# Performance work log

Hardware: AMD Instinct MI355X
Metric: run time of the kernel (lower is better)

## Reference

```python
import jax, jax.numpy as jnp
import numpy as np

N = 50000
E = 800000
IN_DIM = 128
HID = 64
OUT_DIM = 128
NEG_SLOPE = 0.2  # PyG GATConv default


def _add_self_loops(src, dst, edge_attr, n):
    # PyG GATConv(add_self_loops=True) with edge_dim uses fill_value='mean':
    # self-loop edge_attr = mean of edge_attr of incoming edges per node.
    deg = jax.ops.segment_sum(jnp.ones((src.shape[0],), edge_attr.dtype), dst, num_segments=n)
    loop_attr = jax.ops.segment_sum(edge_attr, dst, num_segments=n) / jnp.maximum(deg, 1.0)[:, None]
    loop = jnp.arange(n, dtype=src.dtype)
    return (jnp.concatenate([src, loop]), jnp.concatenate([dst, loop]),
            jnp.concatenate([edge_attr, loop_attr], axis=0))


def _gat_conv(x, src, dst, edge_attr, W, We, a_src, a_dst, a_edge, bias, heads, out_dim, concat, n):
    src, dst, edge_attr = _add_self_loops(src, dst, edge_attr, n)
    h = (x @ W).reshape(n, heads, out_dim)                      # [N,H,D]
    he = (edge_attr @ We).reshape(-1, heads, out_dim)           # [E',H,D]
    alpha_src = jnp.einsum('nhd,hd->nh', h, a_src)
    alpha_dst = jnp.einsum('nhd,hd->nh', h, a_dst)
    alpha_edge = jnp.einsum('ehd,hd->eh', he, a_edge)
    alpha = jax.nn.leaky_relu(alpha_src[src] + alpha_dst[dst] + alpha_edge, NEG_SLOPE)  # [E',H]
    # segment softmax over edges grouped by destination node
    amax = jax.ops.segment_max(alpha, dst, num_segments=n)
    amax = jnp.where(jnp.isfinite(amax), amax, 0.0)
    ex = jnp.exp(alpha - amax[dst])
    denom = jax.ops.segment_sum(ex, dst, num_segments=n)
    coef = ex / (denom[dst] + 1e-16)                            # [E',H]
    msg = h[src] * coef[:, :, None]                             # [E',H,D]
    out = jax.ops.segment_sum(msg, dst, num_segments=n)         # [N,H,D]
    out = out.reshape(n, heads * out_dim) if concat else out.mean(axis=1)
    return out + bias


def setup_inputs() -> dict:
    key = jax.random.key(0)
    ks = jax.random.split(key, 16)
    s = 0.05
    inp = {
        'x': jax.random.normal(ks[0], (N, IN_DIM), jnp.float32),
        'edge_index': jax.random.randint(ks[1], (2, E), 0, N, dtype=jnp.int64),
        'edge_attr': jax.random.normal(ks[2], (E, 2), jnp.float32),
        # gat1: heads=4, concat -> out 4*HID
        'W1': jax.random.normal(ks[3], (IN_DIM, 4 * HID), jnp.float32) * s,
        'We1': jax.random.normal(ks[4], (2, 4 * HID), jnp.float32) * s,
        'asrc1': jax.random.normal(ks[5], (4, HID), jnp.float32) * s,
        'adst1': jax.random.normal(ks[6], (4, HID), jnp.float32) * s,
        'aedge1': jax.random.normal(ks[7], (4, HID), jnp.float32) * s,
        'b1': jnp.zeros((4 * HID,), jnp.float32),
        # gat2: heads=1, concat=False -> out OUT_DIM
        'W2': jax.random.normal(ks[8], (4 * HID, OUT_DIM), jnp.float32) * s,
        'We2': jax.random.normal(ks[9], (2, OUT_DIM), jnp.float32) * s,
        'asrc2': jax.random.normal(ks[10], (1, OUT_DIM), jnp.float32) * s,
        'adst2': jax.random.normal(ks[11], (1, OUT_DIM), jnp.float32) * s,
        'aedge2': jax.random.normal(ks[12], (1, OUT_DIM), jnp.float32) * s,
        'b2': jnp.zeros((OUT_DIM,), jnp.float32),
    }
    return inp


def reference(x, edge_index, edge_attr, W1, We1, asrc1, adst1, aedge1, b1,
              W2, We2, asrc2, adst2, aedge2, b2):
    src, dst = edge_index[0], edge_index[1]
    # dropout layers are identity in eval mode
    h = _gat_conv(x, src, dst, edge_attr, W1, We1, asrc1, adst1, aedge1, b1,
                  heads=4, out_dim=HID, concat=True, n=x.shape[0])
    h = jax.nn.elu(h)
    out = _gat_conv(h, src, dst, edge_attr, W2, We2, asrc2, adst2, aedge2, b2,
                    heads=1, out_dim=OUT_DIM, concat=False, n=x.shape[0])
    return out
```

## Files before the change

kernel.cpp:

```cpp
#include <hip/hip_runtime.h>
#include <hip/hip_bf16.h>

#define NN 50000
#define EE 800000
#define SCAN_B 2048
#define NB ((NN + SCAN_B - 1) / SCAN_B)


typedef short bf16x8 __attribute__((ext_vector_type(8)));
typedef float f32x4  __attribute__((ext_vector_type(4)));

__device__ __forceinline__ float bf2f(unsigned short u) {
    return __uint_as_float(((unsigned)u) << 16);
}
__device__ __forceinline__ unsigned short f2bf(float f) {
    unsigned b = __float_as_uint(f);
    b += 0x7fffu + ((b >> 16) & 1u);
    return (unsigned short)(b >> 16);
}
__device__ __forceinline__ float2 bfpair(unsigned u) {
    return make_float2(__uint_as_float(u << 16), __uint_as_float(u & 0xffff0000u));
}

__global__ void k_prep(const float* __restrict__ We1, const float* __restrict__ ae1,
                       const float* __restrict__ We2, const float* __restrict__ ae2,
                       float* __restrict__ v,
                       const float* __restrict__ W1, unsigned short* __restrict__ W1t,
                       const float* __restrict__ W2, unsigned short* __restrict__ W2t,
                       const int* __restrict__ ei, int* __restrict__ idg,
                       int* __restrict__ rank,
                       const float* __restrict__ x, unsigned short* __restrict__ xb) {
    int bid = blockIdx.x, t = threadIdx.x;
    if (bid == 0) {
        if (t < 8) {
            int c = t >> 2, h = t & 3;
            float s = 0.f;
            for (int d = 0; d < 64; d++) s += We1[c * 256 + h * 64 + d] * ae1[h * 64 + d];
            v[c * 4 + h] = s;
        } else if (t < 10) {
            int c = t - 8;
            float s = 0.f;
            for (int d = 0; d < 128; d++) s += We2[c * 128 + d] * ae2[d];
            v[8 + c] = s;
        }
    } else if (bid <= 256) {
        int idx = (bid - 1) * 256 + t;
        if (idx < 32768) {
            int k = idx >> 8, n = idx & 255;
            W1t[n * 128 + k] = f2bf(W1[idx]);
        } else {
            int i = idx - 32768;
            int k = i >> 7, n = i & 127;
            W2t[n * 256 + k] = f2bf(W2[i]);
        }
    } else if (bid <= 256 + 3125) {
        int e = (bid - 257) * 256 + t;
        if (e < EE) rank[e] = atomicAdd(&idg[ei[EE + e]], 1);
    } else {
        int i = (bid - 3382) * 256 + t;
        if (i < NN * 128 / 4) {
            float4 vv = ((const float4*)x)[i];
            ushort4 o;
            o.x = f2bf(vv.x); o.y = f2bf(vv.y); o.z = f2bf(vv.z); o.w = f2bf(vv.w);
            ((ushort4*)xb)[i] = o;
        }
    }
}

__global__ void k_scan1(const int* __restrict__ idg, int* __restrict__ rowptr,
                        int* __restrict__ bsum) {
    __shared__ int sh[512];
    int t = threadIdx.x;
    int base = blockIdx.x * SCAN_B + t * 4;
    int v[4]; int s = 0;
    #pragma unroll
    for (int j = 0; j < 4; j++) {
        int i = base + j;
        v[j] = (i < NN) ? idg[i] : 0;
        s += v[j];
    }
    sh[t] = s;
    __syncthreads();
    for (int off = 1; off < 512; off <<= 1) {
        int a = (t >= off) ? sh[t - off] : 0;
        __syncthreads();
        sh[t] += a;
        __syncthreads();
    }
    int run = sh[t] - s;
    #pragma unroll
    for (int j = 0; j < 4; j++) {
        int i = base + j;
        if (i < NN) rowptr[i] = run;
        run += v[j];
    }
    if (t == 511) bsum[blockIdx.x] = sh[511];
}

__global__ void k_scan2(const int* __restrict__ bsum, int* __restrict__ boff,
                        int* __restrict__ rowptr) {
    if (threadIdx.x == 0) {
        int acc = 0;
        for (int b = 0; b < NB; b++) { boff[b] = acc; acc += bsum[b]; }
        rowptr[NN] = acc;
    }
}

__global__ void k_scan3(int* __restrict__ rowptr, const int* __restrict__ boff) {
    int t = threadIdx.x;
    int i = blockIdx.x * SCAN_B + t * 4;
    int off = boff[blockIdx.x];
    #pragma unroll
    for (int j = 0; j < 4; j++)
        if (i + j < NN) rowptr[i + j] += off;
}

__global__ void k_scatter(const int* __restrict__ ei, const float* __restrict__ eattr,
                          const int* __restrict__ rowptr, const int* __restrict__ rank,
                          int2* __restrict__ slot) {
    int e = blockIdx.x * blockDim.x + threadIdx.x;
    if (e >= EE) return;
    int s = ei[e], d = ei[EE + e];
    int p = rowptr[d] + rank[e];
    float2 a = ((const float2*)eattr)[e];
    unsigned a0 = f2bf(a.x), a1 = f2bf(a.y);
    slot[p] = make_int2(s, (int)(a0 | (a1 << 16)));
}

template <int K, int NT, int H>
__global__ __launch_bounds__(256) void gemm_mfma(const unsigned short* __restrict__ A,
                                                 const unsigned short* __restrict__ Bt,
                                                 unsigned short* __restrict__ C,
                                                 const float* __restrict__ avs,
                                                 const float* __restrict__ avd,
                                                 float* __restrict__ asrc,
                                                 float* __restrict__ adst,
                                                 int M, int N) {
    int wave = threadIdx.x >> 6, lane = threadIdx.x & 63;
    int l16 = lane & 15, quad = lane >> 4;
    int m0 = blockIdx.y * 128 + wave * 32;
    int n0 = blockIdx.x * (NT * 16);

    f32x4 acc[2][NT];
    #pragma unroll
    for (int mt = 0; mt < 2; mt++)
        #pragma unroll
        for (int nt = 0; nt < NT; nt++)
            acc[mt][nt] = (f32x4){0.f, 0.f, 0.f, 0.f};

    int ar0 = min(m0 + l16, M - 1);
    int ar1 = min(m0 + 16 + l16, M - 1);
    const unsigned short* a0 = A + (size_t)ar0 * K + quad * 8;
    const unsigned short* a1 = A + (size_t)ar1 * K + quad * 8;
    const unsigned short* bp = Bt + (size_t)(n0 + l16) * K + quad * 8;

    #pragma unroll
    for (int k0 = 0; k0 < K; k0 += 32) {
        bf16x8 af0 = *(const bf16x8*)(a0 + k0);
        bf16x8 af1 = *(const bf16x8*)(a1 + k0);
        #pragma unroll
        for (int nt = 0; nt < NT; nt++) {
            bf16x8 bf = *(const bf16x8*)(bp + (size_t)nt * 16 * K + k0);
            acc[0][nt] = __builtin_amdgcn_mfma_f32_16x16x32_bf16(af0, bf, acc[0][nt], 0, 0, 0);
            acc[1][nt] = __builtin_amdgcn_mfma_f32_16x16x32_bf16(af1, bf, acc[1][nt], 0, 0, 0);
        }
    }

    #pragma unroll
    for (int mt = 0; mt < 2; mt++)
        #pragma unroll
        for (int reg = 0; reg < 4; reg++) {
            int row = m0 + mt * 16 + quad * 4 + reg;
            if (row < M) {
                #pragma unroll
                for (int nt = 0; nt < NT; nt++)
                    C[(size_t)row * N + n0 + nt * 16 + l16] = f2bf(acc[mt][nt][reg]);
            }
        }

    float ws[NT], wd[NT];
    #pragma unroll
    for (int nt = 0; nt < NT; nt++) {
        ws[nt] = avs[n0 + nt * 16 + l16];
        wd[nt] = avd[n0 + nt * 16 + l16];
    }
    int hh = n0 >> 6;
    #pragma unroll
    for (int mt = 0; mt < 2; mt++)
        #pragma unroll
        for (int reg = 0; reg < 4; reg++) {
            int row = m0 + mt * 16 + quad * 4 + reg;
            float s1 = 0.f, s2 = 0.f;
            #pragma unroll
            for (int nt = 0; nt < NT; nt++) {
                float c = acc[mt][nt][reg];
                s1 += c * ws[nt];
                s2 += c * wd[nt];
            }
            #pragma unroll
            for (int off = 1; off < 16; off <<= 1) {
                s1 += __shfl_xor(s1, off);
                s2 += __shfl_xor(s2, off);
            }
            if (l16 == 0 && row < M) {
                asrc[row * H + hh] = s1;
                adst[row * H + hh] = s2;
            }
        }
}

__global__ __launch_bounds__(256) void k_agg1(const int* __restrict__ rowptr,
                       const int2* __restrict__ slot, const float* __restrict__ asrc,
                       const float* __restrict__ adst, const float* __restrict__ v,
                       const unsigned short* __restrict__ hb, const float* __restrict__ b1,
                       unsigned short* __restrict__ h2b) {
    int node = blockIdx.x * 4 + (threadIdx.x >> 6);
    if (node >= NN) return;
    int lane = threadIdx.x & 63;
    int q  = lane >> 4;
    int ql = lane & 15;
    int hA = ql >> 3;
    int hB = hA + 2;
    int beg = rowptr[node], end = rowptr[node + 1];
    float pdA = adst[node * 4 + hA], pdB = adst[node * 4 + hB];
    float vA0 = v[hA],     vA1 = v[4 + hA];
    float vB0 = v[hB],     vB1 = v[4 + hB];
    float accA[8] = {}, accB[8] = {};
    float denA = 0.f, denB = 0.f, s0 = 0.f, s1 = 0.f;
    const unsigned short* hbq = hb + ql * 8;

    auto edge = [&](int jj) {
        int2 sl = slot[jj];
        int s = sl.x;
        float2 a = bfpair((unsigned)sl.y);
        float psA = asrc[s * 4 + hA];
        float psB = asrc[s * 4 + hB];
        float alA = psA + pdA + a.x * vA0 + a.y * vA1;
        float alB = psB + pdB + a.x * vB0 + a.y * vB1;
        alA = (alA > 0.f) ? alA : 0.2f * alA;
        alB = (alB > 0.f) ? alB : 0.2f * alB;
        float eA = __expf(alA), eB = __expf(alB);
        s0 += a.x; s1 += a.y;
        denA += eA; denB += eB;
        const uint4* rp = (const uint4*)(hbq + (size_t)s * 256);
        uint4 r0 = rp[0];
        uint4 r1 = rp[16];
        float2 p;
        p = bfpair(r0.x); accA[0] += eA * p.x; accA[1] += eA * p.y;
        p = bfpair(r0.y); accA[2] += eA * p.x; accA[3] += eA * p.y;
        p = bfpair(r0.z); accA[4] += eA * p.x; accA[5] += eA * p.y;
        p = bfpair(r0.w); accA[6] += eA * p.x; accA[7] += eA * p.y;
        p = bfpair(r1.x); accB[0] += eB * p.x; accB[1] += eB * p.y;
        p = bfpair(r1.y); accB[2] += eB * p.x; accB[3] += eB * p.y;
        p = bfpair(r1.z); accB[4] += eB * p.x; accB[5] += eB * p.y;
        p = bfpair(r1.w); accB[6] += eB * p.x; accB[7] += eB * p.y;
    };

    int pb = beg;
    int mend = end - ((end - beg) & 3);
    #pragma unroll 2
    for (; pb < mend; pb += 4) edge(pb + q);
    if (pb + q < end) edge(pb + q);

    #pragma unroll
    for (int k = 0; k < 8; k++) {
        accA[k] += __shfl_down(accA[k], 32);
        accB[k] += __shfl_down(accB[k], 32);
        accA[k] += __shfl_down(accA[k], 16);
        accB[k] += __shfl_down(accB[k], 16);
    }
    denA += __shfl_xor(denA, 16); denA += __shfl_xor(denA, 32);
    denB += __shfl_xor(denB, 16); denB += __shfl_xor(denB, 32);
    s0   += __shfl_xor(s0, 16);   s0   += __shfl_xor(s0, 32);
    s1   += __shfl_xor(s1, 16);   s1   += __shfl_xor(s1, 32);

    float dg = fmaxf((float)(end - beg), 1.0f);
    float alsA = asrc[node * 4 + hA] + pdA + (s0 / dg) * vA0 + (s1 / dg) * vA1;
    float alsB = asrc[node * 4 + hB] + pdB + (s0 / dg) * vB0 + (s1 / dg) * vB1;
    alsA = (alsA > 0.f) ? alsA : 0.2f * alsA;
    alsB = (alsB > 0.f) ? alsB : 0.2f * alsB;
    float exA = __expf(alsA), exB = __expf(alsB);
    denA += exA; denB += exB;

    if (q == 0) {
        const uint4* rp = (const uint4*)(hbq + (size_t)node * 256);
        uint4 r0 = rp[0], r1 = rp[16];
        float2 p;
        p = bfpair(r0.x); accA[0] += exA * p.x; accA[1] += exA * p.y;
        p = bfpair(r0.y); accA[2] += exA * p.x; accA[3] += exA * p.y;
        p = bfpair(r0.z); accA[4] += exA * p.x; accA[5] += exA * p.y;
        p = bfpair(r0.w); accA[6] += exA * p.x; accA[7] += exA * p.y;
        p = bfpair(r1.x); accB[0] += exB * p.x; accB[1] += exB * p.y;
        p = bfpair(r1.y); accB[2] += exB * p.x; accB[3] += exB * p.y;
        p = bfpair(r1.z); accB[4] += exB * p.x; accB[5] += exB * p.y;
        p = bfpair(r1.w); accB[6] += exB * p.x; accB[7] += exB * p.y;
        float invA = 1.f / (denA + 1e-16f);
        float invB = 1.f / (denB + 1e-16f);
        short oa[8], ob[8];
        #pragma unroll
        for (int k = 0; k < 8; k++) {
            float va = accA[k] * invA + b1[ql * 8 + k];
            float vb = accB[k] * invB + b1[128 + ql * 8 + k];
            va = (va > 0.f) ? va : __expf(va) - 1.f;
            vb = (vb > 0.f) ? vb : __expf(vb) - 1.f;
            oa[k] = (short)f2bf(va);
            ob[k] = (short)f2bf(vb);
        }
        bf16x8 vA8 = {oa[0], oa[1], oa[2], oa[3], oa[4], oa[5], oa[6], oa[7]};
        bf16x8 vB8 = {ob[0], ob[1], ob[2], ob[3], ob[4], ob[5], ob[6], ob[7]};
        *(bf16x8*)(h2b + (size_t)node * 256 + ql * 8)       = vA8;
        *(bf16x8*)(h2b + (size_t)node * 256 + 128 + ql * 8) = vB8;
    }
}

__global__ __launch_bounds__(256) void k_agg2(const int* __restrict__ rowptr,
                       const int2* __restrict__ slot, const float* __restrict__ asrc,
                       const float* __restrict__ adst, const float* __restrict__ v,
                       const unsigned short* __restrict__ gb, const float* __restrict__ b2,
                       float* __restrict__ outp) {
    int node = blockIdx.x * 4 + (threadIdx.x >> 6);
    if (node >= NN) return;
    int lane = threadIdx.x & 63;
    int q  = lane >> 4;
    int ql = lane & 15;
    int beg = rowptr[node], end = rowptr[node + 1];
    float ad = adst[node];
    float v0 = v[0], v1 = v[1];
    float acc[8] = {};
    float den = 0.f, s0 = 0.f, s1 = 0.f;
    const unsigned short* gbq = gb + ql * 8;

    auto edge = [&](int jj) {
        int2 sl = slot[jj];
        int s = sl.x;
        float2 a = bfpair((unsigned)sl.y);
        float al = asrc[s] + ad + a.x * v0 + a.y * v1;
        al = (al > 0.f) ? al : 0.2f * al;
        float e = __expf(al);
        s0 += a.x; s1 += a.y; den += e;
        uint4 r = *(const uint4*)(gbq + (size_t)s * 128);
        float2 p;
        p = bfpair(r.x); acc[0] += e * p.x; acc[1] += e * p.y;
        p = bfpair(r.y); acc[2] += e * p.x; acc[3] += e * p.y;
        p = bfpair(r.z); acc[4] += e * p.x; acc[5] += e * p.y;
        p = bfpair(r.w); acc[6] += e * p.x; acc[7] += e * p.y;
    };

    int pb = beg;
    int mend = end - ((end - beg) & 3);
    #pragma unroll 2
    for (; pb < mend; pb += 4) edge(pb + q);
    if (pb + q < end) edge(pb + q);

    #pragma unroll
    for (int k = 0; k < 8; k++) {
        acc[k] += __shfl_down(acc[k], 32);
        acc[k] += __shfl_down(acc[k], 16);
    }
    den += __shfl_xor(den, 16); den += __shfl_xor(den, 32);
    s0  += __shfl_xor(s0, 16);  s0  += __shfl_xor(s0, 32);
    s1  += __shfl_xor(s1, 16);  s1  += __shfl_xor(s1, 32);

    float dg = fmaxf((float)(end - beg), 1.0f);
    float als = asrc[node] + ad + (s0 / dg) * v0 + (s1 / dg) * v1;
    als = (als > 0.f) ? als : 0.2f * als;
    float exs = __expf(als);
    den += exs;

    if (q == 0) {
        uint4 r = *(const uint4*)(gbq + (size_t)node * 128);
        float2 p;
        p = bfpair(r.x); acc[0] += exs * p.x; acc[1] += exs * p.y;
        p = bfpair(r.y); acc[2] += exs * p.x; acc[3] += exs * p.y;
        p = bfpair(r.z); acc[4] += exs * p.x; acc[5] += exs * p.y;
        p = bfpair(r.w); acc[6] += exs * p.x; acc[7] += exs * p.y;
        float inv = 1.f / (den + 1e-16f);
        float4 o0, o1;
        o0.x = acc[0] * inv + b2[ql * 8 + 0];
        o0.y = acc[1] * inv + b2[ql * 8 + 1];
        o0.z = acc[2] * inv + b2[ql * 8 + 2];
        o0.w = acc[3] * inv + b2[ql * 8 + 3];
        o1.x = acc[4] * inv + b2[ql * 8 + 4];
        o1.y = acc[5] * inv + b2[ql * 8 + 5];
        o1.z = acc[6] * inv + b2[ql * 8 + 6];
        o1.w = acc[7] * inv + b2[ql * 8 + 7];
        *(float4*)(outp + (size_t)node * 128 + ql * 8)     = o0;
        *(float4*)(outp + (size_t)node * 128 + ql * 8 + 4) = o1;
    }
}

extern "C" void kernel_launch(void* const* d_in, const int* in_sizes, int n_in,
                              void* d_out, int out_size, void* d_ws, size_t ws_size,
                              hipStream_t stream) {
    const float* x     = (const float*)d_in[0];
    const int*   ei    = (const int*)d_in[1];
    const float* eattr = (const float*)d_in[2];
    const float* W1    = (const float*)d_in[3];
    const float* We1   = (const float*)d_in[4];
    const float* as1   = (const float*)d_in[5];
    const float* ad1   = (const float*)d_in[6];
    const float* ae1   = (const float*)d_in[7];
    const float* b1    = (const float*)d_in[8];
    const float* W2    = (const float*)d_in[9];
    const float* We2   = (const float*)d_in[10];
    const float* as2   = (const float*)d_in[11];
    const float* ad2   = (const float*)d_in[12];
    const float* ae2   = (const float*)d_in[13];
    const float* b2    = (const float*)d_in[14];
    float* out = (float*)d_out;

    int* idg    = (int*)d_ws;
    int* rank   = idg + NN;
    int* rowptr = rank + EE;
    int* bsum   = rowptr + NN + 16;
    int* boff   = bsum + 32;
    int2* slot  = (int2*)(boff + 32);
    float* asrc1 = (float*)(slot + EE);
    float* adst1 = asrc1 + 4 * NN;
    float* asrc2 = adst1 + 4 * NN;
    float* adst2 = asrc2 + NN;
    float* vbuf  = adst2 + NN;
    unsigned short* ub = (unsigned short*)(((uintptr_t)(vbuf + 64) + 63) & ~(uintptr_t)63);
    unsigned short* x_bf  = ub;
    unsigned short* W1t   = x_bf + (size_t)NN * 128;
    unsigned short* W2t   = W1t + 32768;
    unsigned short* h1_bf = W2t + 32768;
    unsigned short* h2_bf = h1_bf + (size_t)NN * 256;
    unsigned short* g2_bf = h2_bf + (size_t)NN * 256;

    hipMemsetAsync(idg, 0, (size_t)NN * sizeof(int), stream);

    k_prep<<<9632, 256, 0, stream>>>(We1, ae1, We2, ae2, vbuf, W1, W1t, W2, W2t,
                                     ei, idg, rank, x, x_bf);
    k_scan1<<<NB, 512, 0, stream>>>(idg, rowptr, bsum);
    k_scan2<<<1, 64, 0, stream>>>(bsum, boff, rowptr);
    k_scan3<<<NB, 512, 0, stream>>>(rowptr, boff);
    k_scatter<<<(EE + 255) / 256, 256, 0, stream>>>(ei, eattr, rowptr, rank, slot);

    gemm_mfma<128, 4, 4><<<dim3(4, (NN + 127) / 128), 256, 0, stream>>>(
        x_bf, W1t, h1_bf, as1, ad1, asrc1, adst1, NN, 256);
    k_agg1<<<(NN + 3) / 4, 256, 0, stream>>>(rowptr, slot, asrc1, adst1, vbuf,
                                             h1_bf, b1, h2_bf);

    gemm_mfma<256, 8, 1><<<dim3(1, (NN + 127) / 128), 256, 0, stream>>>(
        h2_bf, W2t, g2_bf, as2, ad2, asrc2, adst2, NN, 128);
    k_agg2<<<(NN + 3) / 4, 256, 0, stream>>>(rowptr, slot, asrc2, adst2, vbuf + 8,
                                             g2_bf, b2, out);
}
```

Baseline: 339.6 us.

## Remap agg1 lanes to one head per lane and prefetch edge slots in both aggregations

```diff
diff --git a/kernel.cpp b/kernel.cpp
--- a/kernel.cpp
+++ b/kernel.cpp
@@ -217,99 +217,76 @@
     int node = blockIdx.x * 4 + (threadIdx.x >> 6);
     if (node >= NN) return;
     int lane = threadIdx.x & 63;
-    int q  = lane >> 4;
-    int ql = lane & 15;
-    int hA = ql >> 3;
-    int hB = hA + 2;
+    int h2 = lane >> 5;
+    int hl = lane & 31;
+    int hd = hl >> 3;
     int beg = rowptr[node], end = rowptr[node + 1];
-    float pdA = adst[node * 4 + hA], pdB = adst[node * 4 + hB];
-    float vA0 = v[hA],     vA1 = v[4 + hA];
-    float vB0 = v[hB],     vB1 = v[4 + hB];
-    float accA[8] = {}, accB[8] = {};
-    float denA = 0.f, denB = 0.f, s0 = 0.f, s1 = 0.f;
-    const unsigned short* hbq = hb + ql * 8;
-
-    auto edge = [&](int jj) {
-        int2 sl = slot[jj];
-        int s = sl.x;
-        float2 a = bfpair((unsigned)sl.y);
-        float psA = asrc[s * 4 + hA];
-        float psB = asrc[s * 4 + hB];
-        float alA = psA + pdA + a.x * vA0 + a.y * vA1;
-        float alB = psB + pdB + a.x * vB0 + a.y * vB1;
-        alA = (alA > 0.f) ? alA : 0.2f * alA;
-        alB = (alB > 0.f) ? alB : 0.2f * alB;
-        float eA = __expf(alA), eB = __expf(alB);
-        s0 += a.x; s1 += a.y;
-        denA += eA; denB += eB;
-        const uint4* rp = (const uint4*)(hbq + (size_t)s * 256);
-        uint4 r0 = rp[0];
-        uint4 r1 = rp[16];
+    float pd = adst[node * 4 + hd];
+    float vh0 = v[hd], vh1 = v[4 + hd];
+    float acc[8] = {};
+    float den = 0.f, s0 = 0.f, s1 = 0.f;
+    const unsigned short* hbq = hb + hl * 8;
+
+    int cnt = end - beg;
+    int safeLast = max(end - 1, 0);
+    int mend = beg + (cnt & ~1);
+
+    int2 sl0 = slot[min(beg + h2, safeLast)];
+    int2 sl1 = slot[min(beg + 2 + h2, safeLast)];
+
+    auto body = [&](int2 cur) {
+        int s = cur.x;
+        float2 a = bfpair((unsigned)cur.y);
+        float al = asrc[s * 4 + hd] + pd + a.x * vh0 + a.y * vh1;
+        al = (al > 0.f) ? al : 0.2f * al;
+        float e = __expf(al);
+        s0 += a.x; s1 += a.y; den += e;
+        uint4 r = *(const uint4*)(hbq + (size_t)s * 256);
         float2 p;
-        p = bfpair(r0.x); accA[0] += eA * p.x; accA[1] += eA * p.y;
-        p = bfpair(r0.y); accA[2] += eA * p.x; accA[3] += eA * p.y;
-        p = bfpair(r0.z); accA[4] += eA * p.x; accA[5] += eA * p.y;
-        p = bfpair(r0.w); accA[6] += eA * p.x; accA[7] += eA * p.y;
-        p = bfpair(r1.x); accB[0] += eB * p.x; accB[1] += eB * p.y;
-        p = bfpair(r1.y); accB[2] += eB * p.x; accB[3] += eB * p.y;
-        p = bfpair(r1.z); accB[4] += eB * p.x; accB[5] += eB * p.y;
-        p = bfpair(r1.w); accB[6] += eB * p.x; accB[7] += eB * p.y;
+        p = bfpair(r.x); acc[0] += e * p.x; acc[1] += e * p.y;
+        p = bfpair(r.y); acc[2] += e * p.x; acc[3] += e * p.y;
+        p = bfpair(r.z); acc[4] += e * p.x; acc[5] += e * p.y;
+        p = bfpair(r.w); acc[6] += e * p.x; acc[7] += e * p.y;
     };
 
-    int pb = beg;
-    int mend = end - ((end - beg) & 3);
     #pragma unroll 2
-    for (; pb < mend; pb += 4) edge(pb + q);
-    if (pb + q < end) edge(pb + q);
-
-    #pragma unroll
-    for (int k = 0; k < 8; k++) {
-        accA[k] += __shfl_down(accA[k], 32);
-        accB[k] += __shfl_down(accB[k], 32);
-        accA[k] += __shfl_down(accA[k], 16);
-        accB[k] += __shfl_down(accB[k], 16);
-    }
-    denA += __shfl_xor(denA, 16); denA += __shfl_xor(denA, 32);
-    denB += __shfl_xor(denB, 16); denB += __shfl_xor(denB, 32);
-    s0   += __shfl_xor(s0, 16);   s0   += __shfl_xor(s0, 32);
-    s1   += __shfl_xor(s1, 16);   s1   += __shfl_xor(s1, 32);
-
-    float dg = fmaxf((float)(end - beg), 1.0f);
-    float alsA = asrc[node * 4 + hA] + pdA + (s0 / dg) * vA0 + (s1 / dg) * vA1;
-    float alsB = asrc[node * 4 + hB] + pdB + (s0 / dg) * vB0 + (s1 / dg) * vB1;
-    alsA = (alsA > 0.f) ? alsA : 0.2f * alsA;
-    alsB = (alsB > 0.f) ? alsB : 0.2f * alsB;
-    float exA = __expf(alsA), exB = __expf(alsB);
-    denA += exA; denB += exB;
-
-    if (q == 0) {
-        const uint4* rp = (const uint4*)(hbq + (size_t)node * 256);
-        uint4 r0 = rp[0], r1 = rp[16];
+    for (int pb = beg; pb < mend; pb += 2) {
+        int2 cur = sl0;
+        sl0 = sl1;
+        sl1 = slot[min(pb + 4 + h2, safeLast)];
+        body(cur);
+    }
+    if (h2 == 0 && mend < end) body(sl0);
+
+    #pragma unroll
+    for (int k = 0; k < 8; k++) acc[k] += __shfl_down(acc[k], 32);
+    den += __shfl_xor(den, 32);
+    s0  += __shfl_xor(s0, 32);
+    s1  += __shfl_xor(s1, 32);
+
+    float dg = fmaxf((float)cnt, 1.0f);
+    float als = asrc[node * 4 + hd] + pd + (s0 / dg) * vh0 + (s1 / dg) * vh1;
+    als = (als > 0.f) ? als : 0.2f * als;
+    float exs = __expf(als);
+    den += exs;
+
+    if (h2 == 0) {
+        uint4 r = *(const uint4*)(hbq + (size_t)node * 256);
         float2 p;
-        p = bfpair(r0.x); accA[0] += exA * p.x; accA[1] += exA * p.y;
-        p = bfpair(r0.y); accA[2] += exA * p.x; accA[3] += exA * p.y;
-        p = bfpair(r0.z); accA[4] += exA * p.x; accA[5] += exA * p.y;
-        p = bfpair(r0.w); accA[6] += exA * p.x; accA[7] += exA * p.y;
-        p = bfpair(r1.x); accB[0] += exB * p.x; accB[1] += exB * p.y;
-        p = bfpair(r1.y); accB[2] += exB * p.x; accB[3] += exB * p.y;
-        p = bfpair(r1.z); accB[4] += exB * p.x; accB[5] += exB * p.y;
-        p = bfpair(r1.w); accB[6] += exB * p.x; accB[7] += exB * p.y;
-        float invA = 1.f / (denA + 1e-16f);
-        float invB = 1.f / (denB + 1e-16f);
-        short oa[8], ob[8];
+        p = bfpair(r.x); acc[0] += exs * p.x; acc[1] += exs * p.y;
+        p = bfpair(r.y); acc[2] += exs * p.x; acc[3] += exs * p.y;
+        p = bfpair(r.z); acc[4] += exs * p.x; acc[5] += exs * p.y;
+        p = bfpair(r.w); acc[6] += exs * p.x; acc[7] += exs * p.y;
+        float inv = 1.f / (den + 1e-16f);
+        short ov[8];
         #pragma unroll
         for (int k = 0; k < 8; k++) {
-            float va = accA[k] * invA + b1[ql * 8 + k];
-            float vb = accB[k] * invB + b1[128 + ql * 8 + k];
+            float va = acc[k] * inv + b1[hl * 8 + k];
             va = (va > 0.f) ? va : __expf(va) - 1.f;
-            vb = (vb > 0.f) ? vb : __expf(vb) - 1.f;
-            oa[k] = (short)f2bf(va);
-            ob[k] = (short)f2bf(vb);
-        }
-        bf16x8 vA8 = {oa[0], oa[1], oa[2], oa[3], oa[4], oa[5], oa[6], oa[7]};
-        bf16x8 vB8 = {ob[0], ob[1], ob[2], ob[3], ob[4], ob[5], ob[6], ob[7]};
-        *(bf16x8*)(h2b + (size_t)node * 256 + ql * 8)       = vA8;
-        *(bf16x8*)(h2b + (size_t)node * 256 + 128 + ql * 8) = vB8;
+            ov[k] = (short)f2bf(va);
+        }
+        bf16x8 o8 = {ov[0], ov[1], ov[2], ov[3], ov[4], ov[5], ov[6], ov[7]};
+        *(bf16x8*)(h2b + (size_t)node * 256 + hl * 8) = o8;
     }
 }
 
@@ -330,10 +307,16 @@
     float den = 0.f, s0 = 0.f, s1 = 0.f;
     const unsigned short* gbq = gb + ql * 8;
 
-    auto edge = [&](int jj) {
-        int2 sl = slot[jj];
-        int s = sl.x;
-        float2 a = bfpair((unsigned)sl.y);
+    int cnt = end - beg;
+    int safeLast = max(end - 1, 0);
+    int mend = beg + (cnt & ~3);
+
+    int2 sl0 = slot[min(beg + q, safeLast)];
+    int2 sl1 = slot[min(beg + 4 + q, safeLast)];
+
+    auto body = [&](int2 cur) {
+        int s = cur.x;
+        float2 a = bfpair((unsigned)cur.y);
         float al = asrc[s] + ad + a.x * v0 + a.y * v1;
         al = (al > 0.f) ? al : 0.2f * al;
         float e = __expf(al);
@@ -346,11 +329,14 @@
         p = bfpair(r.w); acc[6] += e * p.x; acc[7] += e * p.y;
     };
 
-    int pb = beg;
-    int mend = end - ((end - beg) & 3);
     #pragma unroll 2
-    for (; pb < mend; pb += 4) edge(pb + q);
-    if (pb + q < end) edge(pb + q);
+    for (int pb = beg; pb < mend; pb += 4) {
+        int2 cur = sl0;
+        sl0 = sl1;
+        sl1 = slot[min(pb + 8 + q, safeLast)];
+        body(cur);
+    }
+    if (mend + q < end) body(sl0);
 
     #pragma unroll
     for (int k = 0; k < 8; k++) {
@@ -361,7 +347,7 @@
     s0  += __shfl_xor(s0, 16);  s0  += __shfl_xor(s0, 32);
     s1  += __shfl_xor(s1, 16);  s1  += __shfl_xor(s1, 32);
 
-    float dg = fmaxf((float)(end - beg), 1.0f);
+    float dg = fmaxf((float)cnt, 1.0f);
     float als = asrc[node] + ad + (s0 / dg) * v0 + (s1 / dg) * v1;
     als = (als > 0.f) ? als : 0.2f * als;
     float exs = __expf(als);
```

After: 327.7 us. 1.04x faster.
